# Kernel tuning notes

Measured on AMD Instinct MI355X. Metric: run time of the kernel, lower is better.

The kernel has to match this reference:

```python
import jax, jax.numpy as jnp
import numpy as np

B, N = 65536, 8
OBS0, OBS1, OBS2 = 6, 1024, 7
H, HC, NA = 64, 128, 2


def _glorot(key, shape):
    fan_in = shape[0]
    lim = 1.0 / np.sqrt(fan_in)
    return jax.random.uniform(key, shape, jnp.float32, -lim, lim)


def setup_inputs() -> dict:
    key = jax.random.key(0)
    ks = jax.random.split(key, 24)
    state0 = jax.random.normal(ks[0], (B, OBS0), jnp.float32)
    state1 = jax.random.normal(ks[1], (B, OBS1), jnp.float32)
    state2 = jax.random.normal(ks[2], (B, N, OBS2), jnp.float32)
    keep = (jax.random.uniform(ks[3], (B, N, 1)) > 0.35) | (jnp.arange(N)[None, :, None] == 0)
    state2 = state2 * keep.astype(jnp.float32)
    return {
        "state0": state0, "state1": state1, "state2": state2,
        "W0": _glorot(ks[4], (OBS0, H)), "b0": jnp.zeros((H,), jnp.float32),
        "Wg": _glorot(ks[5], (OBS1, H)), "bg": jnp.zeros((H,), jnp.float32),
        "Ws1": _glorot(ks[6], (OBS2, H)), "bs1": jnp.zeros((H,), jnp.float32),
        "Ws2": _glorot(ks[7], (H, H)), "bs2": jnp.zeros((H,), jnp.float32),
        "Wq": _glorot(ks[8], (H, H)),
        "Wk": _glorot(ks[9], (H, H)),
        "Wv": _glorot(ks[10], (H, H)),
        "Wc1": _glorot(ks[11], (3 * H, HC)), "bc1": jnp.zeros((HC,), jnp.float32),
        "Wc2": _glorot(ks[12], (HC, HC)), "bc2": jnp.zeros((HC,), jnp.float32),
        "Wc3": _glorot(ks[13], (HC, NA)), "bc3": jnp.zeros((NA,), jnp.float32),
    }


def reference(state0, state1, state2,
              W0, b0, Wg, bg, Ws1, bs1, Ws2, bs2,
              Wq, Wk, Wv, Wc1, bc1, Wc2, bc2, Wc3, bc3):
    own_e = jax.nn.relu(state0 @ W0 + b0)                      # [B, 64]
    env_e = jax.nn.relu(state1 @ Wg + bg)                      # [B, 64]
    intru_e = jax.nn.relu(state2 @ Ws1 + bs1)                  # [B, N, 64]
    intru_e = jax.nn.relu(intru_e @ Ws2 + bs2)                 # [B, N, 64]

    q = own_e @ Wq                                             # [B, 64]
    k = intru_e @ Wk                                           # [B, N, 64]
    v = intru_e @ Wv                                           # [B, N, 64]

    # mask: True where the neighbor slot is non-padding (mean over feats != 0)
    mask = jnp.mean(state2, axis=2, keepdims=True) != 0        # [B, N, 1] bool

    score = jnp.einsum('bnd,bd->bn', k, q)[..., None]          # [B, N, 1]
    score_m = jnp.where(mask, score, -jnp.inf)
    alpha = jax.nn.softmax(score_m / np.sqrt(H), axis=1)       # [B, N, 1]
    alpha_m = jnp.where(mask, alpha, 0.0)
    v_att = jnp.sum(v * alpha_m, axis=1)                       # [B, 64]

    concat = jnp.concatenate((own_e, env_e, v_att), axis=1)    # [B, 192]
    h = jax.nn.relu(concat @ Wc1 + bc1)
    h = jax.nn.relu(h @ Wc2 + bc2)
    return jnp.tanh(h @ Wc3 + bc3)                             # [B, n_actions]
```

## Files before the change

### kernel.cpp

```cpp
#include <hip/hip_runtime.h>
#include <math.h>


typedef float f32x4 __attribute__((ext_vector_type(4)));
typedef float f32x4u __attribute__((ext_vector_type(4), aligned(4)));
typedef float f32x2u __attribute__((ext_vector_type(2), aligned(4)));
typedef __bf16 bf16x8 __attribute__((ext_vector_type(8)));
typedef unsigned short u16x8 __attribute__((ext_vector_type(8)));

#define DI __device__ __forceinline__

DI unsigned short f2bf_u(float f) {
  unsigned u = __builtin_bit_cast(unsigned, f);
  u += 0x7fffu + ((u >> 16) & 1u);
  return (unsigned short)(u >> 16);
}
DI float bfu2f(unsigned short s) {
  unsigned u = ((unsigned)s) << 16;
  return __builtin_bit_cast(float, u);
}
DI u16x8 cvt8(f32x4 x, f32x4 y) {
  bf16x8 r;
  r[0] = (__bf16)x[0]; r[1] = (__bf16)x[1]; r[2] = (__bf16)x[2]; r[3] = (__bf16)x[3];
  r[4] = (__bf16)y[0]; r[5] = (__bf16)y[1]; r[6] = (__bf16)y[2]; r[7] = (__bf16)y[3];
  return __builtin_bit_cast(u16x8, r);
}
DI f32x4 mfma16(u16x8 a, u16x8 b, f32x4 c) {
  return __builtin_amdgcn_mfma_f32_16x16x32_bf16(
      __builtin_bit_cast(bf16x8, a), __builtin_bit_cast(bf16x8, b), c, 0, 0, 0);
}


constexpr size_t WS_WGF = 0;
constexpr size_t WS_WS2 = 131072;
constexpr size_t WS_WV  = 139264;
constexpr size_t WS_MQK = 147456;
constexpr size_t WS_WC1 = 155648;
constexpr size_t WS_WC2 = 204800;

__global__ __launch_bounds__(256) void k_prep(
    const float* __restrict__ Wg, const float* __restrict__ Ws2,
    const float* __restrict__ Wv, const float* __restrict__ Wq,
    const float* __restrict__ Wk, const float* __restrict__ Wc1,
    const float* __restrict__ Wc2,
    unsigned short* __restrict__ wgf, unsigned short* __restrict__ ws2f,
    unsigned short* __restrict__ wvf, unsigned short* __restrict__ mqkf,
    unsigned short* __restrict__ wc1f, unsigned short* __restrict__ wc2f) {
  const int idx = blockIdx.x * 256 + threadIdx.x;
  const float* src = nullptr;
  unsigned short* dst;
  int i, ntm, NC;
  bool is_mqk = false;
  if (idx < 65536)      { src = Wg;  dst = wgf;  i = idx;          ntm = 2; NC = 64;  }
  else if (idx < 69632) { src = Ws2; dst = ws2f; i = idx - 65536;  ntm = 2; NC = 64;  }
  else if (idx < 73728) { src = Wv;  dst = wvf;  i = idx - 69632;  ntm = 2; NC = 64;  }
  else if (idx < 77824) { is_mqk = true; dst = mqkf; i = idx - 73728; ntm = 2; NC = 64; }
  else if (idx < 102400){ src = Wc1; dst = wc1f; i = idx - 77824;  ntm = 3; NC = 128; }
  else                  { src = Wc2; dst = wc2f; i = idx - 102400; ntm = 3; NC = 128; }
  const int j = i & 7, ln = (i >> 3) & 63, t2 = i >> 9;
  const int nt = t2 & ((1 << ntm) - 1), kt = t2 >> ntm;
  const int k = kt * 32 + (ln >> 4) * 8 + j, n = nt * 16 + (ln & 15);
  float val;
  if (is_mqk) {
    const f32x4* qp = (const f32x4*)(Wq + k * 64);
    const f32x4* kp = (const f32x4*)(Wk + n * 64);
    float acc = 0.f;
#pragma unroll
    for (int d4 = 0; d4 < 16; ++d4) {
      const f32x4 a = qp[d4], b = kp[d4];
#pragma unroll
      for (int e = 0; e < 4; ++e) acc = fmaf(a[e], b[e], acc);
    }
    val = acc;
  } else {
    val = src[k * NC + n];
  }
  dst[i] = f2bf_u(val);
}

__global__ __launch_bounds__(256, 3) void k_main(
    const float* __restrict__ s0, const float* __restrict__ s1,
    const float* __restrict__ s2,
    const float* __restrict__ W0, const float* __restrict__ b0v,
    const float* __restrict__ bg,
    const float* __restrict__ Ws1, const float* __restrict__ bs1,
    const unsigned short* __restrict__ ws2f, const float* __restrict__ bs2,
    const unsigned short* __restrict__ wvf, const unsigned short* __restrict__ mqkf,
    const unsigned short* __restrict__ wc1f, const float* __restrict__ bc1,
    const unsigned short* __restrict__ wc2f, const float* __restrict__ bc2,
    const float* __restrict__ Wc3, const float* __restrict__ bc3,
    const unsigned short* __restrict__ wgf,
    float* __restrict__ out) {
  __shared__ __align__(16) char smem[54272];
  u16x8* EF = (u16x8*)smem;
  unsigned short* EFs = (unsigned short*)smem;
  u16x8* H1F = (u16x8*)smem;
  unsigned short* H1Fs = (unsigned short*)smem;
  float* H2 = (float*)(smem + 8192);
  u16x8* CF = (u16x8*)(smem + 32768);
  unsigned short* CFs = (unsigned short*)(smem + 32768);
  float* QK = (float*)(smem + 45056);
  f32x4* RED4 = (f32x4*)(smem + 45056);
  u16x8* SEF = (u16x8*)(smem + 45056);
  float* SC = (float*)(smem + 53248);

  const int tid = threadIdx.x;
  const int lane = tid & 63, wave = tid >> 6;
  const int lo = lane & 15, q = lane >> 4;
  const int bbase = blockIdx.x * 32;

  const int bl8 = tid >> 3, n8 = tid & 7;
  const float* s2p = s2 + ((size_t)(bbase + bl8) * 8 + n8) * 7;
  const f32x4u x03 = *(const f32x4u*)s2p;
  const f32x2u x45 = *(const f32x2u*)(s2p + 4);
  const float x6 = s2p[6];
  const float* s0p = s0 + (size_t)(bbase + bl8) * 6;
  const f32x4u y03 = *(const f32x4u*)s0p;
  const f32x2u y45 = *(const f32x2u*)(s0p + 4);

  const int p = wave & 1, emt = wave >> 1;
  {
    const float* arow =
        s1 + (size_t)(bbase + emt * 16 + lo) * 1024 + p * 512 + q * 8;
    const u16x8* wp = (const u16x8*)wgf + p * 4096 + lane;
    f32x4 acc0 = {}, acc1 = {}, acc2 = {}, acc3 = {};
    f32x4 a0 = *(const f32x4*)arow, a1 = *(const f32x4*)(arow + 4);
    u16x8 b0 = wp[0], b1 = wp[64], b2 = wp[128], b3 = wp[192];
    for (int ks = 0; ks < 16; ++ks) {
      const f32x4 ca0 = a0, ca1 = a1;
      const u16x8 cb0 = b0, cb1 = b1, cb2 = b2, cb3 = b3;
      if (ks < 15) {
        const float* ap = arow + (ks + 1) * 32;
        a0 = *(const f32x4*)ap;
        a1 = *(const f32x4*)(ap + 4);
        const u16x8* bp = wp + (ks + 1) * 256;
        b0 = bp[0]; b1 = bp[64]; b2 = bp[128]; b3 = bp[192];
      }
      const u16x8 af = cvt8(ca0, ca1);
      acc0 = mfma16(af, cb0, acc0);
      acc1 = mfma16(af, cb1, acc1);
      acc2 = mfma16(af, cb2, acc2);
      acc3 = mfma16(af, cb3, acc3);
    }
    if (p) {
      RED4[0 * 128 + emt * 64 + lane] = acc0;
      RED4[1 * 128 + emt * 64 + lane] = acc1;
      RED4[2 * 128 + emt * 64 + lane] = acc2;
      RED4[3 * 128 + emt * 64 + lane] = acc3;
    }
    __syncthreads();
    if (!p) {
      acc0 += RED4[0 * 128 + emt * 64 + lane];
      acc1 += RED4[1 * 128 + emt * 64 + lane];
      acc2 += RED4[2 * 128 + emt * 64 + lane];
      acc3 += RED4[3 * 128 + emt * 64 + lane];
      const f32x4 av[4] = {acc0, acc1, acc2, acc3};
#pragma unroll
      for (int nt = 0; nt < 4; ++nt) {
        const float bias = bg[nt * 16 + lo];
        const int h = nt * 16 + lo;
#pragma unroll
        for (int ri = 0; ri < 4; ++ri) {
          const float v = fmaxf(av[nt][ri] + bias, 0.f);
          CFs[((emt * 6 + 2 + (h >> 5)) * 64 +
               ((((h >> 3) & 3) << 4) | (q * 4 + ri))) * 8 + (h & 7)] = f2bf_u(v);
        }
      }
    }
  }

  bool maskreg;
  {
    float xv[7] = {x03[0], x03[1], x03[2], x03[3], x45[0], x45[1], x6};
    const float sum = xv[0] + xv[1] + xv[2] + xv[3] + xv[4] + xv[5] + xv[6];
    maskreg = (sum != 0.f);
    const int mt = tid >> 4, rl = tid & 15;
#pragma unroll
    for (int c = 0; c < 8; ++c) {
      float a[8];
#pragma unroll
      for (int i = 0; i < 8; ++i) a[i] = bs1[c * 8 + i];
#pragma unroll
      for (int j = 0; j < 7; ++j) {
        const float* wr = Ws1 + j * 64 + c * 8;
#pragma unroll
        for (int i = 0; i < 8; ++i) a[i] = fmaf(xv[j], wr[i], a[i]);
      }
      u16x8 pk;
#pragma unroll
      for (int i = 0; i < 8; ++i) pk[i] = f2bf_u(fmaxf(a[i], 0.f));
      EF[(mt * 2 + (c >> 2)) * 64 + (((c & 3) << 4) | rl)] = pk;
    }
  }
  __syncthreads();

  {
    u16x8 Bf[4][2];
#pragma unroll
    for (int nt = 0; nt < 4; ++nt)
#pragma unroll
      for (int kt = 0; kt < 2; ++kt)
        Bf[nt][kt] = ((const u16x8*)ws2f)[(kt * 4 + nt) * 64 + lane];
    float bias[4];
#pragma unroll
    for (int nt = 0; nt < 4; ++nt) bias[nt] = bs2[nt * 16 + lo];
#pragma unroll
    for (int mi = 0; mi < 4; ++mi) {
      const int mt = wave * 4 + mi;
      const u16x8 A0 = EF[(mt * 2 + 0) * 64 + lane];
      const u16x8 A1 = EF[(mt * 2 + 1) * 64 + lane];
      f32x4 acc[4] = {};
#pragma unroll
      for (int nt = 0; nt < 4; ++nt) {
        acc[nt] = mfma16(A0, Bf[nt][0], acc[nt]);
        acc[nt] = mfma16(A1, Bf[nt][1], acc[nt]);
      }
#pragma unroll
      for (int nt = 0; nt < 4; ++nt) {
        const int h = nt * 16 + lo;
#pragma unroll
        for (int ri = 0; ri < 4; ++ri) {
          const float v = fmaxf(acc[nt][ri] + bias[nt], 0.f);
          const int rr = mt * 16 + q * 4 + ri;
          EFs[((mt * 2 + (h >> 5)) * 64 + ((((h >> 3) & 3) << 4) | (rr & 15))) * 8 +
              (h & 7)] = f2bf_u(v);
        }
      }
    }
  }
  __syncthreads();

  {
    const int mt = bl8 >> 4, fl = ((n8 & 3) << 4) | (bl8 & 15), kt = n8 >> 2;
    const float yv[6] = {y03[0], y03[1], y03[2], y03[3], y45[0], y45[1]};
    float a[8];
#pragma unroll
    for (int i = 0; i < 8; ++i) a[i] = b0v[n8 * 8 + i];
#pragma unroll
    for (int j = 0; j < 6; ++j) {
      const float* wr = W0 + j * 64 + n8 * 8;
#pragma unroll
      for (int i = 0; i < 8; ++i) a[i] = fmaf(yv[j], wr[i], a[i]);
    }
    u16x8 pk;
#pragma unroll
    for (int i = 0; i < 8; ++i) pk[i] = f2bf_u(fmaxf(a[i], 0.f));
    CF[(mt * 6 + kt) * 64 + fl] = pk;
  }
  __syncthreads();

  {
#pragma unroll
    for (int pp = 0; pp < 2; ++pp) {
      const int pr = wave * 2 + pp, mt = pr >> 2, nt = pr & 3;
      const u16x8 A0 = CF[(mt * 6 + 0) * 64 + lane];
      const u16x8 A1 = CF[(mt * 6 + 1) * 64 + lane];
      const u16x8 B0 = ((const u16x8*)mqkf)[(0 * 4 + nt) * 64 + lane];
      const u16x8 B1 = ((const u16x8*)mqkf)[(1 * 4 + nt) * 64 + lane];
      f32x4 acc = {};
      acc = mfma16(A0, B0, acc);
      acc = mfma16(A1, B1, acc);
#pragma unroll
      for (int ri = 0; ri < 4; ++ri)
        QK[(mt * 16 + q * 4 + ri) * 64 + nt * 16 + lo] = acc[ri];
    }
  }
  __syncthreads();

  {
    const int r = tid, bl = r >> 3, mt = r >> 4, rl = r & 15;
    float dot = 0.f;
#pragma unroll
    for (int c = 0; c < 8; ++c) {
      const u16x8 e = EF[(mt * 2 + (c >> 2)) * 64 + (((c & 3) << 4) | rl)];
      const float* qkp = QK + bl * 64 + c * 8;
      const f32x4 qa = *(const f32x4*)(qkp);
      const f32x4 qb = *(const f32x4*)(qkp + 4);
#pragma unroll
      for (int i = 0; i < 4; ++i) dot = fmaf(bfu2f(e[i]), qa[i], dot);
#pragma unroll
      for (int i = 0; i < 4; ++i) dot = fmaf(bfu2f(e[4 + i]), qb[i], dot);
    }
    SC[r] = maskreg ? dot * 0.125f : -1e30f;
  }
  __syncthreads();

  if (tid < 32) {
    float s[8];
#pragma unroll
    for (int n = 0; n < 8; ++n) s[n] = SC[tid * 8 + n];
    float mx = s[0];
#pragma unroll
    for (int n = 1; n < 8; ++n) mx = fmaxf(mx, s[n]);
    float e[8], sum = 0.f;
#pragma unroll
    for (int n = 0; n < 8; ++n) { e[n] = __expf(s[n] - mx); sum += e[n]; }
    const float inv = 1.f / sum;
#pragma unroll
    for (int n = 0; n < 8; ++n) SC[tid * 8 + n] = e[n] * inv;
  }
  __syncthreads();

  {
    float al[8];
#pragma unroll
    for (int n = 0; n < 8; ++n) al[n] = SC[bl8 * 8 + n];
    float a[8] = {0.f, 0.f, 0.f, 0.f, 0.f, 0.f, 0.f, 0.f};
#pragma unroll
    for (int n = 0; n < 8; ++n) {
      const int rr = bl8 * 8 + n;
      const u16x8 e =
          EF[((rr >> 4) * 2 + (n8 >> 2)) * 64 + (((n8 & 3) << 4) | (rr & 15))];
#pragma unroll
      for (int i = 0; i < 8; ++i) a[i] = fmaf(al[n], bfu2f(e[i]), a[i]);
    }
    u16x8 pk;
#pragma unroll
    for (int i = 0; i < 8; ++i) pk[i] = f2bf_u(a[i]);
    SEF[((bl8 >> 4) * 2 + (n8 >> 2)) * 64 + (((n8 & 3) << 4) | (bl8 & 15))] = pk;
  }
  __syncthreads();

  {
#pragma unroll
    for (int pp = 0; pp < 2; ++pp) {
      const int pr = wave * 2 + pp, mt = pr >> 2, nt = pr & 3;
      const u16x8 A0 = SEF[(mt * 2 + 0) * 64 + lane];
      const u16x8 A1 = SEF[(mt * 2 + 1) * 64 + lane];
      const u16x8 B0 = ((const u16x8*)wvf)[(0 * 4 + nt) * 64 + lane];
      const u16x8 B1 = ((const u16x8*)wvf)[(1 * 4 + nt) * 64 + lane];
      f32x4 acc = {};
      acc = mfma16(A0, B0, acc);
      acc = mfma16(A1, B1, acc);
      const int h = nt * 16 + lo;
#pragma unroll
      for (int ri = 0; ri < 4; ++ri) {
        const int rr = mt * 16 + q * 4 + ri;
        CFs[((mt * 6 + 4 + (h >> 5)) * 64 + ((((h >> 3) & 3) << 4) | (rr & 15))) * 8 +
            (h & 7)] = f2bf_u(acc[ri]);
      }
    }
  }
  __syncthreads();

  {
    const int mt = wave & 1, ntb = (wave >> 1) * 4;
    u16x8 A[6];
#pragma unroll
    for (int kt = 0; kt < 6; ++kt) A[kt] = CF[(mt * 6 + kt) * 64 + lane];
#pragma unroll
    for (int ni = 0; ni < 4; ++ni) {
      const int nt = ntb + ni;
      f32x4 acc = {};
#pragma unroll
      for (int kt = 0; kt < 6; ++kt) {
        const u16x8 Bf = ((const u16x8*)wc1f)[(kt * 8 + nt) * 64 + lane];
        acc = mfma16(A[kt], Bf, acc);
      }
      const float bias = bc1[nt * 16 + lo];
      const int h = nt * 16 + lo;
#pragma unroll
      for (int ri = 0; ri < 4; ++ri) {
        const float v = fmaxf(acc[ri] + bias, 0.f);
        const int rr = mt * 16 + q * 4 + ri;
        H1Fs[((mt * 4 + (h >> 5)) * 64 + ((((h >> 3) & 3) << 4) | (rr & 15))) * 8 +
             (h & 7)] = f2bf_u(v);
      }
    }
  }
  __syncthreads();

  {
    const int mt = wave & 1, ntb = (wave >> 1) * 4;
    u16x8 A[4];
#pragma unroll
    for (int kt = 0; kt < 4; ++kt) A[kt] = H1F[(mt * 4 + kt) * 64 + lane];
#pragma unroll
    for (int ni = 0; ni < 4; ++ni) {
      const int nt = ntb + ni;
      f32x4 acc = {};
#pragma unroll
      for (int kt = 0; kt < 4; ++kt) {
        const u16x8 Bf = ((const u16x8*)wc2f)[(kt * 8 + nt) * 64 + lane];
        acc = mfma16(A[kt], Bf, acc);
      }
      const float bias = bc2[nt * 16 + lo];
#pragma unroll
      for (int ri = 0; ri < 4; ++ri)
        H2[(mt * 16 + q * 4 + ri) * 132 + nt * 16 + lo] =
            fmaxf(acc[ri] + bias, 0.f);
    }
  }
  __syncthreads();

  {
    const int kq = n8 >> 1, a = n8 & 1;
    const f32x4* h4 = (const f32x4*)(H2 + bl8 * 132 + kq * 32);
    const float* wr = Wc3 + kq * 64;
    float acc = 0.f;
#pragma unroll
    for (int j4 = 0; j4 < 8; ++j4) {
      const f32x4 hv = h4[j4];
#pragma unroll
      for (int e = 0; e < 4; ++e) acc = fmaf(hv[e], wr[(j4 * 4 + e) * 2 + a], acc);
    }
    acc += __shfl_down(acc, 2);
    acc += __shfl_down(acc, 4);
    if (kq == 0) out[(size_t)(bbase + bl8) * 2 + a] = tanhf(acc + bc3[a]);
  }
}

extern "C" void kernel_launch(void* const* d_in, const int* in_sizes, int n_in,
                              void* d_out, int out_size, void* d_ws, size_t ws_size,
                              hipStream_t stream) {
  const float* s0  = (const float*)d_in[0];
  const float* s1  = (const float*)d_in[1];
  const float* s2  = (const float*)d_in[2];
  const float* W0  = (const float*)d_in[3];
  const float* b0  = (const float*)d_in[4];
  const float* Wg  = (const float*)d_in[5];
  const float* bg  = (const float*)d_in[6];
  const float* Ws1 = (const float*)d_in[7];
  const float* bs1 = (const float*)d_in[8];
  const float* Ws2 = (const float*)d_in[9];
  const float* bs2 = (const float*)d_in[10];
  const float* Wq  = (const float*)d_in[11];
  const float* Wk  = (const float*)d_in[12];
  const float* Wv  = (const float*)d_in[13];
  const float* Wc1 = (const float*)d_in[14];
  const float* bc1 = (const float*)d_in[15];
  const float* Wc2 = (const float*)d_in[16];
  const float* bc2 = (const float*)d_in[17];
  const float* Wc3 = (const float*)d_in[18];
  const float* bc3 = (const float*)d_in[19];

  char* ws = (char*)d_ws;
  unsigned short* wgf  = (unsigned short*)(ws + WS_WGF);
  unsigned short* ws2f = (unsigned short*)(ws + WS_WS2);
  unsigned short* wvf  = (unsigned short*)(ws + WS_WV);
  unsigned short* mqkf = (unsigned short*)(ws + WS_MQK);
  unsigned short* wc1f = (unsigned short*)(ws + WS_WC1);
  unsigned short* wc2f = (unsigned short*)(ws + WS_WC2);

  hipLaunchKernelGGL(k_prep, dim3(464), dim3(256), 0, stream, Wg, Ws2, Wv, Wq,
                     Wk, Wc1, Wc2, wgf, ws2f, wvf, mqkf, wc1f, wc2f);
  hipLaunchKernelGGL(k_main, dim3(2048), dim3(256), 0, stream, s0, s1, s2, W0,
                     b0, bg, Ws1, bs1, ws2f, bs2, wvf, mqkf, wc1f, bc1, wc2f,
                     bc2, Wc3, bc3, wgf, (float*)d_out);
}
```

Before: 460.2 us.

## Split env GEMM into separate kernel writing bf16 env features to workspace

Moves the large state1 @ Wg GEMM out of the fused main kernel into its own kernel. The new kernel processes 16 rows per block across 4 waves, each covering a quarter of K, with all A loads issued up front and a four-way LDS reduction. It writes bf16 env features to workspace, and the remaining kernel reads them into its concat buffer. The intent is better memory-level parallelism for the bandwidth-bound 256MB state1 stream, with no intra-block serialization against the rest of the network. The cost is an extra launch and an 8MB workspace round-trip.

```diff
diff --git a/kernel.cpp b/kernel.cpp
--- a/kernel.cpp
+++ b/kernel.cpp
@@ -37,6 +37,7 @@
 constexpr size_t WS_MQK = 147456;
 constexpr size_t WS_WC1 = 155648;
 constexpr size_t WS_WC2 = 204800;
+constexpr size_t WS_ENV = 237568;
 
 __global__ __launch_bounds__(256) void k_prep(
     const float* __restrict__ Wg, const float* __restrict__ Ws2,
@@ -78,20 +79,63 @@
   dst[i] = f2bf_u(val);
 }
 
-__global__ __launch_bounds__(256, 3) void k_main(
-    const float* __restrict__ s0, const float* __restrict__ s1,
-    const float* __restrict__ s2,
+__global__ __launch_bounds__(256, 3) void k_env(
+    const float* __restrict__ s1, const float* __restrict__ bg,
+    const unsigned short* __restrict__ wgf, unsigned short* __restrict__ env) {
+  __shared__ __align__(16) f32x4 RED[16 * 64];
+  const int tid = threadIdx.x, lane = tid & 63, wave = tid >> 6;
+  const int lo = lane & 15, q = lane >> 4;
+  const int r0 = blockIdx.x * 16;
+  const float* arow = s1 + (size_t)(r0 + lo) * 1024 + wave * 256 + q * 8;
+
+  f32x4 A[8][2];
+#pragma unroll
+  for (int ks = 0; ks < 8; ++ks) {
+    A[ks][0] = *(const f32x4*)(arow + ks * 32);
+    A[ks][1] = *(const f32x4*)(arow + ks * 32 + 4);
+  }
+  const u16x8* wp = (const u16x8*)wgf + lane;
+  u16x8 Bb[2][4];
+#pragma unroll
+  for (int nt = 0; nt < 4; ++nt) Bb[0][nt] = wp[((wave * 8) * 4 + nt) * 64];
+  f32x4 acc[4] = {};
+#pragma unroll
+  for (int ks = 0; ks < 8; ++ks) {
+    const int cur = ks & 1;
+    if (ks < 7) {
+#pragma unroll
+      for (int nt = 0; nt < 4; ++nt)
+        Bb[cur ^ 1][nt] = wp[((wave * 8 + ks + 1) * 4 + nt) * 64];
+    }
+    const u16x8 af = cvt8(A[ks][0], A[ks][1]);
+#pragma unroll
+    for (int nt = 0; nt < 4; ++nt) acc[nt] = mfma16(af, Bb[cur][nt], acc[nt]);
+  }
+#pragma unroll
+  for (int nt = 0; nt < 4; ++nt) RED[(wave * 4 + nt) * 64 + lane] = acc[nt];
+  __syncthreads();
+  f32x4 s = RED[(0 * 4 + wave) * 64 + lane];
+#pragma unroll
+  for (int p = 1; p < 4; ++p) s += RED[(p * 4 + wave) * 64 + lane];
+  const float bias = bg[wave * 16 + lo];
+#pragma unroll
+  for (int ri = 0; ri < 4; ++ri)
+    env[(size_t)(r0 + q * 4 + ri) * 64 + wave * 16 + lo] =
+        f2bf_u(fmaxf(s[ri] + bias, 0.f));
+}
+
+__global__ __launch_bounds__(256, 3) void k_rest(
+    const float* __restrict__ s0, const float* __restrict__ s2,
+    const unsigned short* __restrict__ env,
     const float* __restrict__ W0, const float* __restrict__ b0v,
-    const float* __restrict__ bg,
     const float* __restrict__ Ws1, const float* __restrict__ bs1,
     const unsigned short* __restrict__ ws2f, const float* __restrict__ bs2,
     const unsigned short* __restrict__ wvf, const unsigned short* __restrict__ mqkf,
     const unsigned short* __restrict__ wc1f, const float* __restrict__ bc1,
     const unsigned short* __restrict__ wc2f, const float* __restrict__ bc2,
     const float* __restrict__ Wc3, const float* __restrict__ bc3,
-    const unsigned short* __restrict__ wgf,
     float* __restrict__ out) {
-  __shared__ __align__(16) char smem[54272];
+  __shared__ __align__(16) char smem[53248];
   u16x8* EF = (u16x8*)smem;
   unsigned short* EFs = (unsigned short*)smem;
   u16x8* H1F = (u16x8*)smem;
@@ -99,10 +143,9 @@
   float* H2 = (float*)(smem + 8192);
   u16x8* CF = (u16x8*)(smem + 32768);
   unsigned short* CFs = (unsigned short*)(smem + 32768);
+  float* SC = (float*)(smem + 36864);
   float* QK = (float*)(smem + 45056);
-  f32x4* RED4 = (f32x4*)(smem + 45056);
   u16x8* SEF = (u16x8*)(smem + 45056);
-  float* SC = (float*)(smem + 53248);
 
   const int tid = threadIdx.x;
   const int lane = tid & 63, wave = tid >> 6;
@@ -117,57 +160,7 @@
   const float* s0p = s0 + (size_t)(bbase + bl8) * 6;
   const f32x4u y03 = *(const f32x4u*)s0p;
   const f32x2u y45 = *(const f32x2u*)(s0p + 4);
-
-  const int p = wave & 1, emt = wave >> 1;
-  {
-    const float* arow =
-        s1 + (size_t)(bbase + emt * 16 + lo) * 1024 + p * 512 + q * 8;
-    const u16x8* wp = (const u16x8*)wgf + p * 4096 + lane;
-    f32x4 acc0 = {}, acc1 = {}, acc2 = {}, acc3 = {};
-    f32x4 a0 = *(const f32x4*)arow, a1 = *(const f32x4*)(arow + 4);
-    u16x8 b0 = wp[0], b1 = wp[64], b2 = wp[128], b3 = wp[192];
-    for (int ks = 0; ks < 16; ++ks) {
-      const f32x4 ca0 = a0, ca1 = a1;
-      const u16x8 cb0 = b0, cb1 = b1, cb2 = b2, cb3 = b3;
-      if (ks < 15) {
-        const float* ap = arow + (ks + 1) * 32;
-        a0 = *(const f32x4*)ap;
-        a1 = *(const f32x4*)(ap + 4);
-        const u16x8* bp = wp + (ks + 1) * 256;
-        b0 = bp[0]; b1 = bp[64]; b2 = bp[128]; b3 = bp[192];
-      }
-      const u16x8 af = cvt8(ca0, ca1);
-      acc0 = mfma16(af, cb0, acc0);
-      acc1 = mfma16(af, cb1, acc1);
-      acc2 = mfma16(af, cb2, acc2);
-      acc3 = mfma16(af, cb3, acc3);
-    }
-    if (p) {
-      RED4[0 * 128 + emt * 64 + lane] = acc0;
-      RED4[1 * 128 + emt * 64 + lane] = acc1;
-      RED4[2 * 128 + emt * 64 + lane] = acc2;
-      RED4[3 * 128 + emt * 64 + lane] = acc3;
-    }
-    __syncthreads();
-    if (!p) {
-      acc0 += RED4[0 * 128 + emt * 64 + lane];
-      acc1 += RED4[1 * 128 + emt * 64 + lane];
-      acc2 += RED4[2 * 128 + emt * 64 + lane];
-      acc3 += RED4[3 * 128 + emt * 64 + lane];
-      const f32x4 av[4] = {acc0, acc1, acc2, acc3};
-#pragma unroll
-      for (int nt = 0; nt < 4; ++nt) {
-        const float bias = bg[nt * 16 + lo];
-        const int h = nt * 16 + lo;
-#pragma unroll
-        for (int ri = 0; ri < 4; ++ri) {
-          const float v = fmaxf(av[nt][ri] + bias, 0.f);
-          CFs[((emt * 6 + 2 + (h >> 5)) * 64 +
-               ((((h >> 3) & 3) << 4) | (q * 4 + ri))) * 8 + (h & 7)] = f2bf_u(v);
-        }
-      }
-    }
-  }
+  const u16x8 ev = *(const u16x8*)(env + (size_t)(bbase + bl8) * 64 + n8 * 8);
 
   bool maskreg;
   {
@@ -246,6 +239,7 @@
 #pragma unroll
     for (int i = 0; i < 8; ++i) pk[i] = f2bf_u(fmaxf(a[i], 0.f));
     CF[(mt * 6 + kt) * 64 + fl] = pk;
+    CF[(mt * 6 + 2 + kt) * 64 + fl] = ev;
   }
   __syncthreads();
 
@@ -441,10 +435,12 @@
   unsigned short* mqkf = (unsigned short*)(ws + WS_MQK);
   unsigned short* wc1f = (unsigned short*)(ws + WS_WC1);
   unsigned short* wc2f = (unsigned short*)(ws + WS_WC2);
+  unsigned short* env  = (unsigned short*)(ws + WS_ENV);
 
   hipLaunchKernelGGL(k_prep, dim3(464), dim3(256), 0, stream, Wg, Ws2, Wv, Wq,
                      Wk, Wc1, Wc2, wgf, ws2f, wvf, mqkf, wc1f, wc2f);
-  hipLaunchKernelGGL(k_main, dim3(2048), dim3(256), 0, stream, s0, s1, s2, W0,
-                     b0, bg, Ws1, bs1, ws2f, bs2, wvf, mqkf, wc1f, bc1, wc2f,
-                     bc2, Wc3, bc3, wgf, (float*)d_out);
-}
+  hipLaunchKernelGGL(k_env, dim3(4096), dim3(256), 0, stream, s1, bg, wgf, env);
+  hipLaunchKernelGGL(k_rest, dim3(2048), dim3(256), 0, stream, s0, s2, env, W0,
+                     b0, Ws1, bs1, ws2f, bs2, wvf, mqkf, wc1f, bc1, wc2f, bc2,
+                     Wc3, bc3, (float*)d_out);
+}
```

Result: slower. 469.5 us (+2.0%).
